# Kernel tuning notes

Measured on AMD Instinct MI355X. Metric: run time of the kernel, lower is better.

The kernel has to match this reference:

```python
import jax, jax.numpy as jnp
import numpy as np

N_USER = 100_000
N_ITEM = 50_000
C = 128
E = 600_000
L = 2          # num_layers
NN = 2         # num_layers_nn (MLP depth inside GINConv)
LN_EPS = 1e-5


def _layernorm(x, g, b):
    # PyG LayerNorm(mode='node'): normalize each node over channels, affine
    m = jnp.mean(x, axis=-1, keepdims=True)
    v = jnp.mean((x - m) ** 2, axis=-1, keepdims=True)
    return (x - m) * jax.lax.rsqrt(v + LN_EPS) * g + b


def _mlp(x, W, b):
    # GINConv inner MLP: [Linear -> ReLU] * NN
    for i in range(NN):
        x = jax.nn.relu(x @ W[i] + b[i])
    return x


def setup_inputs() -> dict:
    key = jax.random.key(0)
    ks = jax.random.split(key, 10)
    s = 1.0 / np.sqrt(C)
    edge_ui = jnp.stack([
        jax.random.randint(ks[0], (E,), 0, N_USER, dtype=jnp.int32),  # src: user
        jax.random.randint(ks[1], (E,), 0, N_ITEM, dtype=jnp.int32),  # dst: item
    ])
    edge_iu = jnp.stack([
        jax.random.randint(ks[2], (E,), 0, N_ITEM, dtype=jnp.int32),  # src: item
        jax.random.randint(ks[3], (E,), 0, N_USER, dtype=jnp.int32),  # dst: user
    ])
    return {
        "x_user": jax.random.normal(ks[4], (N_USER, C), dtype=jnp.float32),
        "x_item": jax.random.normal(ks[5], (N_ITEM, C), dtype=jnp.float32),
        "W_init": jax.random.normal(ks[6], (2, C, C), dtype=jnp.float32) * s,
        "b_init": jnp.zeros((2, C), dtype=jnp.float32),
        "mlp_W": jax.random.normal(ks[7], (L, 2, NN, C, C), dtype=jnp.float32) * s,
        "mlp_b": jnp.zeros((L, 2, NN, C), dtype=jnp.float32),
        "eps": jnp.full((L, 2), 1e-5, dtype=jnp.float32),  # train_eps=True, init eps=1e-5
        "ln_g": jnp.ones((L, 2, C), dtype=jnp.float32),
        "ln_b": jnp.zeros((L, 2, C), dtype=jnp.float32),
        "edge_ui": edge_ui,
        "edge_iu": edge_iu,
    }


def reference(x_user, x_item, W_init, b_init, mlp_W, mlp_b, eps, ln_g, ln_b,
              edge_ui, edge_iu):
    # Initial per-node-type projection (LazyLinear)
    xu = x_user @ W_init[0] + b_init[0]
    xi = x_item @ W_init[1] + b_init[1]
    for l in range(L):
        # GINConv per edge type; HeteroConv(aggr='sum') trivially reduces since
        # each node type is targeted by exactly one edge type here.
        agg_i = jax.ops.segment_sum(xu[edge_ui[0]], edge_ui[1], num_segments=N_ITEM)
        agg_u = jax.ops.segment_sum(xi[edge_iu[0]], edge_iu[1], num_segments=N_USER)
        # edge_type index 0 = (user->item), 1 = (item->user)
        new_i = _mlp((1.0 + eps[l, 0]) * xi + agg_i, mlp_W[l, 0], mlp_b[l, 0])
        new_u = _mlp((1.0 + eps[l, 1]) * xu + agg_u, mlp_W[l, 1], mlp_b[l, 1])
        # node_type index 0 = user, 1 = item
        xu = jax.nn.relu(_layernorm(new_u, ln_g[l, 0], ln_b[l, 0]))
        xi = jax.nn.relu(_layernorm(new_i, ln_g[l, 1], ln_b[l, 1]))
    return (xu, xi)
```

## Files before the change

kernel.cpp:

```cpp
#include <hip/hip_runtime.h>
#include <cstdint>
#include <cstddef>

#define N_USER 100000
#define N_ITEM 50000
#define CDIM   128
#define NEDGE  600000
#define N_SEG  (N_ITEM + N_USER)
#define NB_SCAN ((N_SEG + 255) / 256)

#define FILL_EPB 2048
#define FILL_NCHUNK ((NEDGE + FILL_EPB - 1) / FILL_EPB)
#define SLICE_DIV ((N_SEG + 7) / 8)

typedef __bf16 bf16_t;
typedef bf16_t bfvec8 __attribute__((ext_vector_type(8)));
typedef bf16_t bfvec4 __attribute__((ext_vector_type(4)));
typedef float  f32x4  __attribute__((ext_vector_type(4)));

#define LDW 136

__global__ __launch_bounds__(256) void prep_weights(
    const float* __restrict__ W_init, const float* __restrict__ mlp_W,
    bf16_t* __restrict__ wtg)
{
    int m  = blockIdx.x >> 6;
    int it = blockIdx.x & 63;
    const float* src = (m < 2) ? (W_init + (size_t)m * 16384)
                               : (mlp_W + (size_t)(m - 2) * 16384);
    int e = it * 256 + threadIdx.x;
    int n = e >> 7, k = e & 127;
    wtg[(size_t)m * 16384 + e] = (bf16_t)src[k * 128 + n];
}

template <int NT>
static __device__ inline void stage_wbf(bf16_t* Wt, const bf16_t* __restrict__ Wg, int tid) {
    #pragma unroll
    for (int c = tid; c < 2048; c += NT) {
        int n = c >> 4, koff = (c & 15) * 8;
        *reinterpret_cast<bfvec8*>(&Wt[n * LDW + koff]) =
            *reinterpret_cast<const bfvec8*>(&Wg[n * 128 + koff]);
    }
}

__global__ __launch_bounds__(512) void gemm_init(
    const float* __restrict__ X,
    const bf16_t* __restrict__ Wg,
    const float* __restrict__ B,
    bf16_t* __restrict__ Y, int M)
{
    __shared__ __align__(16) bf16_t Wt[128 * LDW];
    const int tid = threadIdx.x;
    stage_wbf<512>(Wt, Wg, tid);
    __syncthreads();

    const int wave = tid >> 6, lane = tid & 63;
    const int quad = lane >> 4, ln16 = lane & 15;
    const int row_l = wave * 16 + ln16;
    const int rowg = blockIdx.x * 128 + row_l;
    const int rowc = rowg < M ? rowg : 0;

    bfvec8 xb[4];
    const float* xp = X + (size_t)rowc * CDIM + quad * 8;
    #pragma unroll
    for (int kc = 0; kc < 4; ++kc) {
        f32x4 lo = *reinterpret_cast<const f32x4*>(xp + kc * 32);
        f32x4 hi = *reinterpret_cast<const f32x4*>(xp + kc * 32 + 4);
        #pragma unroll
        for (int j = 0; j < 4; ++j) {
            xb[kc][j]     = (bf16_t)lo[j];
            xb[kc][j + 4] = (bf16_t)hi[j];
        }
    }

    f32x4 acc[8];
    #pragma unroll
    for (int t = 0; t < 8; ++t) acc[t] = (f32x4){0.f, 0.f, 0.f, 0.f};
    #pragma unroll
    for (int t = 0; t < 8; ++t) {
        const bf16_t* wp = &Wt[(t * 16 + ln16) * LDW + quad * 8];
        #pragma unroll
        for (int kc = 0; kc < 4; ++kc) {
            bfvec8 wv = *reinterpret_cast<const bfvec8*>(wp + kc * 32);
            acc[t] = __builtin_amdgcn_mfma_f32_16x16x32_bf16(wv, xb[kc], acc[t], 0, 0, 0);
        }
    }

    if (rowg < M) {
        #pragma unroll
        for (int t = 0; t < 8; ++t) {
            f32x4 bv = *reinterpret_cast<const f32x4*>(&B[t * 16 + quad * 4]);
            bfvec4 o;
            #pragma unroll
            for (int r = 0; r < 4; ++r) o[r] = (bf16_t)(acc[t][r] + bv[r]);
            *reinterpret_cast<bfvec4*>(&Y[(size_t)rowg * CDIM + t * 16 + quad * 4]) = o;
        }
    }
}

__global__ __launch_bounds__(256) void zero_i32(int* __restrict__ p, int n)
{
    int i = blockIdx.x * 256 + threadIdx.x;
    if (i < n) p[i] = 0;
}

__global__ __launch_bounds__(256) void hist_rank(
    const int* __restrict__ edge_ui, const int* __restrict__ edge_iu,
    int* __restrict__ deg, int2* __restrict__ rank2)
{
    int i = blockIdx.x * 256 + threadIdx.x;
    if (i >= NEDGE) return;
    int r0 = atomicAdd(&deg[edge_ui[NEDGE + i]], 1);
    int r1 = atomicAdd(&deg[N_ITEM + edge_iu[NEDGE + i]], 1);
    rank2[i] = make_int2(r0, r1);
}

__global__ __launch_bounds__(256) void block_scan(
    int* __restrict__ off, int* __restrict__ bsum, int n)
{
    __shared__ int sh[256];
    int tid = threadIdx.x;
    int i = blockIdx.x * 256 + tid;
    int v = (i < n) ? off[i] : 0;
    sh[tid] = v;
    __syncthreads();
    #pragma unroll
    for (int d = 1; d < 256; d <<= 1) {
        int t = (tid >= d) ? sh[tid - d] : 0;
        __syncthreads();
        sh[tid] += t;
        __syncthreads();
    }
    if (i < n) off[i] = sh[tid] - v;
    if (tid == 255) bsum[blockIdx.x] = sh[255];
}

__global__ __launch_bounds__(1024) void scan_bsums(int* __restrict__ bsum)
{
    __shared__ int sh[1024];
    int tid = threadIdx.x;
    int v = (tid < NB_SCAN) ? bsum[tid] : 0;
    sh[tid] = v;
    __syncthreads();
    #pragma unroll
    for (int d = 1; d < 1024; d <<= 1) {
        int t = (tid >= d) ? sh[tid - d] : 0;
        __syncthreads();
        sh[tid] += t;
        __syncthreads();
    }
    if (tid < NB_SCAN) bsum[tid] = sh[tid] - v;
    if (tid == 1023) bsum[NB_SCAN] = sh[1023];
}

__global__ __launch_bounds__(256) void add_offsets(
    int* __restrict__ off, const int* __restrict__ bsum, int n)
{
    int i = blockIdx.x * 256 + threadIdx.x;
    if (i < n) off[i] += bsum[i >> 8];
    else if (i == n) off[n] = bsum[NB_SCAN];
}

__global__ __launch_bounds__(256) void fill_sliced(
    const int* __restrict__ edge_ui, const int* __restrict__ edge_iu,
    const int* __restrict__ off, const int2* __restrict__ rank2,
    int* __restrict__ srcbuf)
{
    const int r = blockIdx.x & 7;
    const int chunk = blockIdx.x >> 3;
    const int base = chunk * FILL_EPB + threadIdx.x;
    #pragma unroll
    for (int j = 0; j < FILL_EPB / 256; ++j) {
        int i = base + j * 256;
        if (i < NEDGE) {
            int d0 = edge_ui[NEDGE + i];
            int d1 = edge_iu[NEDGE + i] + N_ITEM;
            int2 rk = rank2[i];
            if (d0 / SLICE_DIV == r)
                srcbuf[off[d0] + rk.x] = edge_ui[i];
            if (d1 / SLICE_DIV == r)
                srcbuf[off[d1] + rk.y] = edge_iu[i];
        }
    }
}

__global__ __launch_bounds__(256) void gather_both(
    const bf16_t* __restrict__ xu, const bf16_t* __restrict__ xi,
    const float* __restrict__ eps2,
    const int* __restrict__ off_all, const int* __restrict__ srcbuf,
    bf16_t* __restrict__ ti, bf16_t* __restrict__ tu)
{
    const int gBI = (N_ITEM + 3) / 4;
    int b = blockIdx.x;
    bool isItem = b < gBI;
    int wave = threadIdx.x >> 6;
    int node = (isItem ? b : b - gBI) * 4 + wave;
    int n = isItem ? N_ITEM : N_USER;
    if (node >= n) return;

    const bfvec8* F = reinterpret_cast<const bfvec8*>(isItem ? xu : xi);
    const bfvec8* X = reinterpret_cast<const bfvec8*>(isItem ? xi : xu);
    const int* off = isItem ? off_all : off_all + N_ITEM;
    bfvec8* out = reinterpret_cast<bfvec8*>(isItem ? ti : tu);
    float s = 1.f + (isItem ? eps2[0] : eps2[1]);

    int lane = threadIdx.x & 63;
    int grp  = lane >> 4;
    int l16  = lane & 15;
    int start = off[node], end = off[node + 1];

    float acc[8];
    #pragma unroll
    for (int j = 0; j < 8; ++j) acc[j] = 0.f;

    int e = start + grp;
    for (; e + 12 < end; e += 16) {
        int s0 = srcbuf[e];
        int s1 = srcbuf[e + 4];
        int s2 = srcbuf[e + 8];
        int s3 = srcbuf[e + 12];
        bfvec8 v0 = F[(size_t)s0 * 16 + l16];
        bfvec8 v1 = F[(size_t)s1 * 16 + l16];
        bfvec8 v2 = F[(size_t)s2 * 16 + l16];
        bfvec8 v3 = F[(size_t)s3 * 16 + l16];
        #pragma unroll
        for (int j = 0; j < 8; ++j)
            acc[j] += ((float)v0[j] + (float)v1[j]) + ((float)v2[j] + (float)v3[j]);
    }
    for (; e + 4 < end; e += 8) {
        int s0 = srcbuf[e];
        int s1 = srcbuf[e + 4];
        bfvec8 v0 = F[(size_t)s0 * 16 + l16];
        bfvec8 v1 = F[(size_t)s1 * 16 + l16];
        #pragma unroll
        for (int j = 0; j < 8; ++j) acc[j] += (float)v0[j] + (float)v1[j];
    }
    for (; e < end; e += 4) {
        bfvec8 v = F[(size_t)srcbuf[e] * 16 + l16];
        #pragma unroll
        for (int j = 0; j < 8; ++j) acc[j] += (float)v[j];
    }

    #pragma unroll
    for (int j = 0; j < 8; ++j) {
        acc[j] += __shfl_xor(acc[j], 16, 64);
        acc[j] += __shfl_xor(acc[j], 32, 64);
    }

    if (grp == 0) {
        bfvec8 xv = X[(size_t)node * 16 + l16];
        bfvec8 o;
        #pragma unroll
        for (int j = 0; j < 8; ++j) o[j] = (bf16_t)(s * (float)xv[j] + acc[j]);
        out[(size_t)node * 16 + l16] = o;
    }
}

__global__ __launch_bounds__(512) void mlp_ln_both(
    const bf16_t* __restrict__ ti, const bf16_t* __restrict__ tu,
    const bf16_t* __restrict__ wg,
    const float* __restrict__ mlpb,
    const float* __restrict__ lng,
    const float* __restrict__ lnb,
    bf16_t* __restrict__ xib, bf16_t* __restrict__ xub,
    float* __restrict__ xif, float* __restrict__ xuf,
    int f32out)
{
    __shared__ __align__(16) bf16_t Wt[128 * LDW];
    __shared__ __align__(16) bf16_t At[128 * LDW];

    const int gBI = (N_ITEM + 127) / 128;
    int b = blockIdx.x;
    bool isItem = b < gBI;
    const bf16_t* X = isItem ? ti : tu;
    bf16_t* Yb      = isItem ? xib : xub;
    float*  Yf      = isItem ? xif : xuf;
    int M  = isItem ? N_ITEM : N_USER;
    int bx = isItem ? b : b - gBI;
    const bf16_t* W1 = wg + (isItem ? 0 : 2) * 16384;
    const bf16_t* W2 = W1 + 16384;
    const float* B1 = mlpb + (isItem ? 0 : 2) * 128;
    const float* B2 = B1 + 128;
    const float* G  = lng + (isItem ? 128 : 0);
    const float* Bb = lnb + (isItem ? 128 : 0);

    const int tid = threadIdx.x;
    stage_wbf<512>(Wt, W1, tid);
    __syncthreads();

    const int wave = tid >> 6, lane = tid & 63;
    const int quad = lane >> 4, ln16 = lane & 15;
    const int row_l = wave * 16 + ln16;
    const int rowg = bx * 128 + row_l;
    const int rowc = rowg < M ? rowg : 0;

    bfvec8 xb[4];
    const bf16_t* xp = X + (size_t)rowc * CDIM + quad * 8;
    #pragma unroll
    for (int kc = 0; kc < 4; ++kc)
        xb[kc] = *reinterpret_cast<const bfvec8*>(xp + kc * 32);

    f32x4 acc[8];
    #pragma unroll
    for (int t = 0; t < 8; ++t) acc[t] = (f32x4){0.f, 0.f, 0.f, 0.f};
    #pragma unroll
    for (int t = 0; t < 8; ++t) {
        const bf16_t* wp = &Wt[(t * 16 + ln16) * LDW + quad * 8];
        #pragma unroll
        for (int kc = 0; kc < 4; ++kc) {
            bfvec8 wv = *reinterpret_cast<const bfvec8*>(wp + kc * 32);
            acc[t] = __builtin_amdgcn_mfma_f32_16x16x32_bf16(wv, xb[kc], acc[t], 0, 0, 0);
        }
    }

    #pragma unroll
    for (int t = 0; t < 8; ++t) {
        f32x4 bv = *reinterpret_cast<const f32x4*>(&B1[t * 16 + quad * 4]);
        bfvec4 o;
        #pragma unroll
        for (int r = 0; r < 4; ++r) {
            float v = acc[t][r] + bv[r];
            o[r] = (bf16_t)(v > 0.f ? v : 0.f);
        }
        *reinterpret_cast<bfvec4*>(&At[row_l * LDW + t * 16 + quad * 4]) = o;
    }
    __syncthreads();
    stage_wbf<512>(Wt, W2, tid);
    __syncthreads();

    bfvec8 hb[4];
    #pragma unroll
    for (int kc = 0; kc < 4; ++kc)
        hb[kc] = *reinterpret_cast<const bfvec8*>(&At[row_l * LDW + kc * 32 + quad * 8]);

    #pragma unroll
    for (int t = 0; t < 8; ++t) acc[t] = (f32x4){0.f, 0.f, 0.f, 0.f};
    #pragma unroll
    for (int t = 0; t < 8; ++t) {
        const bf16_t* wp = &Wt[(t * 16 + ln16) * LDW + quad * 8];
        #pragma unroll
        for (int kc = 0; kc < 4; ++kc) {
            bfvec8 wv = *reinterpret_cast<const bfvec8*>(wp + kc * 32);
            acc[t] = __builtin_amdgcn_mfma_f32_16x16x32_bf16(wv, hb[kc], acc[t], 0, 0, 0);
        }
    }

    #pragma unroll
    for (int t = 0; t < 8; ++t) {
        f32x4 bv = *reinterpret_cast<const f32x4*>(&B2[t * 16 + quad * 4]);
        #pragma unroll
        for (int r = 0; r < 4; ++r) {
            float v = acc[t][r] + bv[r];
            acc[t][r] = v > 0.f ? v : 0.f;
        }
    }

    float sm = 0.f;
    #pragma unroll
    for (int t = 0; t < 8; ++t)
        #pragma unroll
        for (int r = 0; r < 4; ++r) sm += acc[t][r];
    sm += __shfl_xor(sm, 16, 64);
    sm += __shfl_xor(sm, 32, 64);
    float mean = sm * (1.f / 128.f);
    float sq = 0.f;
    #pragma unroll
    for (int t = 0; t < 8; ++t)
        #pragma unroll
        for (int r = 0; r < 4; ++r) { float d = acc[t][r] - mean; sq += d * d; }
    sq += __shfl_xor(sq, 16, 64);
    sq += __shfl_xor(sq, 32, 64);
    float rs = rsqrtf(sq * (1.f / 128.f) + 1e-5f);

    if (rowg < M) {
        if (f32out) {
            #pragma unroll
            for (int t = 0; t < 8; ++t) {
                f32x4 g4 = *reinterpret_cast<const f32x4*>(&G[t * 16 + quad * 4]);
                f32x4 b4 = *reinterpret_cast<const f32x4*>(&Bb[t * 16 + quad * 4]);
                f32x4 y;
                #pragma unroll
                for (int r = 0; r < 4; ++r) {
                    float v = (acc[t][r] - mean) * rs * g4[r] + b4[r];
                    y[r] = v > 0.f ? v : 0.f;
                }
                *reinterpret_cast<f32x4*>(&Yf[(size_t)rowg * CDIM + t * 16 + quad * 4]) = y;
            }
        } else {
            #pragma unroll
            for (int t = 0; t < 8; ++t) {
                f32x4 g4 = *reinterpret_cast<const f32x4*>(&G[t * 16 + quad * 4]);
                f32x4 b4 = *reinterpret_cast<const f32x4*>(&Bb[t * 16 + quad * 4]);
                bfvec4 y;
                #pragma unroll
                for (int r = 0; r < 4; ++r) {
                    float v = (acc[t][r] - mean) * rs * g4[r] + b4[r];
                    y[r] = (bf16_t)(v > 0.f ? v : 0.f);
                }
                *reinterpret_cast<bfvec4*>(&Yb[(size_t)rowg * CDIM + t * 16 + quad * 4]) = y;
            }
        }
    }
}

extern "C" void kernel_launch(void* const* d_in, const int* in_sizes, int n_in,
                              void* d_out, int out_size, void* d_ws, size_t ws_size,
                              hipStream_t stream)
{
    const float* x_user = (const float*)d_in[0];
    const float* x_item = (const float*)d_in[1];
    const float* W_init = (const float*)d_in[2];
    const float* b_init = (const float*)d_in[3];
    const float* mlp_W  = (const float*)d_in[4];
    const float* mlp_b  = (const float*)d_in[5];
    const float* eps    = (const float*)d_in[6];
    const float* ln_g   = (const float*)d_in[7];
    const float* ln_b   = (const float*)d_in[8];
    const int* edge_ui  = (const int*)d_in[9];
    const int* edge_iu  = (const int*)d_in[10];

    float* xuf = (float*)d_out;
    float* xif = xuf + (size_t)N_USER * CDIM;

    char* w = (char*)d_ws;
    bf16_t* xub = (bf16_t*)w;
    bf16_t* xib = xub + (size_t)N_USER * CDIM;
    bf16_t* tub = xib + (size_t)N_ITEM * CDIM;
    bf16_t* tib = tub + (size_t)N_USER * CDIM;
    int* off_all = (int*)(tib + (size_t)N_ITEM * CDIM);
    int* bsum    = off_all + (N_SEG + 4);
    int* srcbuf  = bsum + (NB_SCAN + 2);
    bf16_t* wtg  = (bf16_t*)(srcbuf + 2 * NEDGE);

    int2* rank2 = (int2*)tub;

    const int gU = (N_USER + 127) / 128;
    const int gI = (N_ITEM + 127) / 128;
    const int gSeg = (N_SEG + 256) / 256;
    const int gE = (NEDGE + 255) / 256;
    const int gGather = (N_ITEM + 3) / 4 + (N_USER + 3) / 4;

    prep_weights<<<640, 256, 0, stream>>>(W_init, mlp_W, wtg);

    zero_i32<<<(N_SEG + 255) / 256, 256, 0, stream>>>(off_all, N_SEG);
    hist_rank<<<gE, 256, 0, stream>>>(edge_ui, edge_iu, off_all, rank2);
    block_scan<<<NB_SCAN, 256, 0, stream>>>(off_all, bsum, N_SEG);
    scan_bsums<<<1, 1024, 0, stream>>>(bsum);
    add_offsets<<<gSeg, 256, 0, stream>>>(off_all, bsum, N_SEG);
    fill_sliced<<<FILL_NCHUNK * 8, 256, 0, stream>>>(edge_ui, edge_iu, off_all, rank2, srcbuf);

    gemm_init<<<gU, 512, 0, stream>>>(x_user, wtg,         b_init,       xub, N_USER);
    gemm_init<<<gI, 512, 0, stream>>>(x_item, wtg + 16384, b_init + 128, xib, N_ITEM);

    for (int l = 0; l < 2; ++l) {
        gather_both<<<gGather, 256, 0, stream>>>(
            xub, xib, eps + 2 * l, off_all, srcbuf, tib, tub);
        mlp_ln_both<<<gI + gU, 512, 0, stream>>>(
            tib, tub, wtg + (size_t)(2 + l * 4) * 16384, mlp_b + l * 4 * 128,
            ln_g + l * 2 * 128, ln_b + l * 2 * 128,
            xib, xub, xif, xuf, (l == 1) ? 1 : 0);
    }
}
```

Measured before the change: 467.7 us.

## Fuse neighbor gather into MLP+LayerNorm kernel via shared-memory staging

Merges the per-node gather/aggregation kernel into the MLP+LayerNorm kernel. Each 128-row block now gathers its own rows' neighbor sums directly into the shared-memory A tile before the MFMA GEMMs, and uses ping-pong buffers across the two layers. This removes the intermediate bf16 write and re-read of the aggregated features and two kernel launches. The cost is that each wave now walks 16 nodes serially with less parallelism and memory-level overlap than the old one-node-per-wave launch, and the 512-thread blocks carry the larger shared footprint during the latency-bound gather phase.

```diff
diff --git a/kernel.cpp b/kernel.cpp
--- a/kernel.cpp
+++ b/kernel.cpp
@@ -184,85 +184,15 @@
     }
 }
 
-__global__ __launch_bounds__(256) void gather_both(
-    const bf16_t* __restrict__ xu, const bf16_t* __restrict__ xi,
+__global__ __launch_bounds__(512) void gin_layer(
+    const bf16_t* __restrict__ xu_in, const bf16_t* __restrict__ xi_in,
     const float* __restrict__ eps2,
     const int* __restrict__ off_all, const int* __restrict__ srcbuf,
-    bf16_t* __restrict__ ti, bf16_t* __restrict__ tu)
-{
-    const int gBI = (N_ITEM + 3) / 4;
-    int b = blockIdx.x;
-    bool isItem = b < gBI;
-    int wave = threadIdx.x >> 6;
-    int node = (isItem ? b : b - gBI) * 4 + wave;
-    int n = isItem ? N_ITEM : N_USER;
-    if (node >= n) return;
-
-    const bfvec8* F = reinterpret_cast<const bfvec8*>(isItem ? xu : xi);
-    const bfvec8* X = reinterpret_cast<const bfvec8*>(isItem ? xi : xu);
-    const int* off = isItem ? off_all : off_all + N_ITEM;
-    bfvec8* out = reinterpret_cast<bfvec8*>(isItem ? ti : tu);
-    float s = 1.f + (isItem ? eps2[0] : eps2[1]);
-
-    int lane = threadIdx.x & 63;
-    int grp  = lane >> 4;
-    int l16  = lane & 15;
-    int start = off[node], end = off[node + 1];
-
-    float acc[8];
-    #pragma unroll
-    for (int j = 0; j < 8; ++j) acc[j] = 0.f;
-
-    int e = start + grp;
-    for (; e + 12 < end; e += 16) {
-        int s0 = srcbuf[e];
-        int s1 = srcbuf[e + 4];
-        int s2 = srcbuf[e + 8];
-        int s3 = srcbuf[e + 12];
-        bfvec8 v0 = F[(size_t)s0 * 16 + l16];
-        bfvec8 v1 = F[(size_t)s1 * 16 + l16];
-        bfvec8 v2 = F[(size_t)s2 * 16 + l16];
-        bfvec8 v3 = F[(size_t)s3 * 16 + l16];
-        #pragma unroll
-        for (int j = 0; j < 8; ++j)
-            acc[j] += ((float)v0[j] + (float)v1[j]) + ((float)v2[j] + (float)v3[j]);
-    }
-    for (; e + 4 < end; e += 8) {
-        int s0 = srcbuf[e];
-        int s1 = srcbuf[e + 4];
-        bfvec8 v0 = F[(size_t)s0 * 16 + l16];
-        bfvec8 v1 = F[(size_t)s1 * 16 + l16];
-        #pragma unroll
-        for (int j = 0; j < 8; ++j) acc[j] += (float)v0[j] + (float)v1[j];
-    }
-    for (; e < end; e += 4) {
-        bfvec8 v = F[(size_t)srcbuf[e] * 16 + l16];
-        #pragma unroll
-        for (int j = 0; j < 8; ++j) acc[j] += (float)v[j];
-    }
-
-    #pragma unroll
-    for (int j = 0; j < 8; ++j) {
-        acc[j] += __shfl_xor(acc[j], 16, 64);
-        acc[j] += __shfl_xor(acc[j], 32, 64);
-    }
-
-    if (grp == 0) {
-        bfvec8 xv = X[(size_t)node * 16 + l16];
-        bfvec8 o;
-        #pragma unroll
-        for (int j = 0; j < 8; ++j) o[j] = (bf16_t)(s * (float)xv[j] + acc[j]);
-        out[(size_t)node * 16 + l16] = o;
-    }
-}
-
-__global__ __launch_bounds__(512) void mlp_ln_both(
-    const bf16_t* __restrict__ ti, const bf16_t* __restrict__ tu,
     const bf16_t* __restrict__ wg,
     const float* __restrict__ mlpb,
     const float* __restrict__ lng,
     const float* __restrict__ lnb,
-    bf16_t* __restrict__ xib, bf16_t* __restrict__ xub,
+    bf16_t* __restrict__ yib, bf16_t* __restrict__ yub,
     float* __restrict__ xif, float* __restrict__ xuf,
     int f32out)
 {
@@ -272,11 +202,16 @@
     const int gBI = (N_ITEM + 127) / 128;
     int b = blockIdx.x;
     bool isItem = b < gBI;
-    const bf16_t* X = isItem ? ti : tu;
-    bf16_t* Yb      = isItem ? xib : xub;
-    float*  Yf      = isItem ? xif : xuf;
     int M  = isItem ? N_ITEM : N_USER;
     int bx = isItem ? b : b - gBI;
+
+    const bfvec8* F = reinterpret_cast<const bfvec8*>(isItem ? xu_in : xi_in);
+    const bfvec8* X = reinterpret_cast<const bfvec8*>(isItem ? xi_in : xu_in);
+    const int* off = isItem ? off_all : off_all + N_ITEM;
+    bf16_t* Yb     = isItem ? yib : yub;
+    float*  Yf     = isItem ? xif : xuf;
+    float s = 1.f + (isItem ? eps2[0] : eps2[1]);
+
     const bf16_t* W1 = wg + (isItem ? 0 : 2) * 16384;
     const bf16_t* W2 = W1 + 16384;
     const float* B1 = mlpb + (isItem ? 0 : 2) * 128;
@@ -286,19 +221,77 @@
 
     const int tid = threadIdx.x;
     stage_wbf<512>(Wt, W1, tid);
-    __syncthreads();
 
     const int wave = tid >> 6, lane = tid & 63;
     const int quad = lane >> 4, ln16 = lane & 15;
+    const int rowBase = bx * 128;
+
+    for (int rr = 0; rr < 16; ++rr) {
+        int rowl = wave * 16 + rr;
+        int node = rowBase + rowl;
+        float acc[8];
+        #pragma unroll
+        for (int j = 0; j < 8; ++j) acc[j] = 0.f;
+
+        if (node < M) {
+            int start = off[node], end = off[node + 1];
+            int e = start + quad;
+            for (; e + 12 < end; e += 16) {
+                int s0 = srcbuf[e];
+                int s1 = srcbuf[e + 4];
+                int s2 = srcbuf[e + 8];
+                int s3 = srcbuf[e + 12];
+                bfvec8 v0 = F[(size_t)s0 * 16 + ln16];
+                bfvec8 v1 = F[(size_t)s1 * 16 + ln16];
+                bfvec8 v2 = F[(size_t)s2 * 16 + ln16];
+                bfvec8 v3 = F[(size_t)s3 * 16 + ln16];
+                #pragma unroll
+                for (int j = 0; j < 8; ++j)
+                    acc[j] += ((float)v0[j] + (float)v1[j]) + ((float)v2[j] + (float)v3[j]);
+            }
+            for (; e + 4 < end; e += 8) {
+                int s0 = srcbuf[e];
+                int s1 = srcbuf[e + 4];
+                bfvec8 v0 = F[(size_t)s0 * 16 + ln16];
+                bfvec8 v1 = F[(size_t)s1 * 16 + ln16];
+                #pragma unroll
+                for (int j = 0; j < 8; ++j) acc[j] += (float)v0[j] + (float)v1[j];
+            }
+            for (; e < end; e += 4) {
+                bfvec8 v = F[(size_t)srcbuf[e] * 16 + ln16];
+                #pragma unroll
+                for (int j = 0; j < 8; ++j) acc[j] += (float)v[j];
+            }
+        }
+
+        #pragma unroll
+        for (int j = 0; j < 8; ++j) {
+            acc[j] += __shfl_xor(acc[j], 16, 64);
+            acc[j] += __shfl_xor(acc[j], 32, 64);
+        }
+
+        if (quad == 0) {
+            bfvec8 o;
+            if (node < M) {
+                bfvec8 xv = X[(size_t)node * 16 + ln16];
+                #pragma unroll
+                for (int j = 0; j < 8; ++j) o[j] = (bf16_t)(s * (float)xv[j] + acc[j]);
+            } else {
+                #pragma unroll
+                for (int j = 0; j < 8; ++j) o[j] = (bf16_t)0.f;
+            }
+            *reinterpret_cast<bfvec8*>(&At[rowl * LDW + ln16 * 8]) = o;
+        }
+    }
+    __syncthreads();
+
     const int row_l = wave * 16 + ln16;
-    const int rowg = bx * 128 + row_l;
-    const int rowc = rowg < M ? rowg : 0;
+    const int rowg = rowBase + row_l;
 
     bfvec8 xb[4];
-    const bf16_t* xp = X + (size_t)rowc * CDIM + quad * 8;
     #pragma unroll
     for (int kc = 0; kc < 4; ++kc)
-        xb[kc] = *reinterpret_cast<const bfvec8*>(xp + kc * 32);
+        xb[kc] = *reinterpret_cast<const bfvec8*>(&At[row_l * LDW + kc * 32 + quad * 8]);
 
     f32x4 acc[8];
     #pragma unroll
@@ -438,7 +431,6 @@
     const int gI = (N_ITEM + 127) / 128;
     const int gSeg = (N_SEG + 256) / 256;
     const int gE = (NEDGE + 255) / 256;
-    const int gGather = (N_ITEM + 3) / 4 + (N_USER + 3) / 4;
 
     prep_weights<<<640, 256, 0, stream>>>(W_init, mlp_W, wtg);
 
@@ -452,12 +444,12 @@
     gemm_init<<<gU, 512, 0, stream>>>(x_user, wtg,         b_init,       xub, N_USER);
     gemm_init<<<gI, 512, 0, stream>>>(x_item, wtg + 16384, b_init + 128, xib, N_ITEM);
 
-    for (int l = 0; l < 2; ++l) {
-        gather_both<<<gGather, 256, 0, stream>>>(
-            xub, xib, eps + 2 * l, off_all, srcbuf, tib, tub);
-        mlp_ln_both<<<gI + gU, 512, 0, stream>>>(
-            tib, tub, wtg + (size_t)(2 + l * 4) * 16384, mlp_b + l * 4 * 128,
-            ln_g + l * 2 * 128, ln_b + l * 2 * 128,
-            xib, xub, xif, xuf, (l == 1) ? 1 : 0);
-    }
-}
+    gin_layer<<<gI + gU, 512, 0, stream>>>(
+        xub, xib, eps, off_all, srcbuf,
+        wtg + (size_t)2 * 16384, mlp_b, ln_g, ln_b,
+        tib, tub, xif, xuf, 0);
+    gin_layer<<<gI + gU, 512, 0, stream>>>(
+        tub, tib, eps + 2, off_all, srcbuf,
+        wtg + (size_t)6 * 16384, mlp_b + 4 * 128, ln_g + 2 * 128, ln_b + 2 * 128,
+        nullptr, nullptr, xif, xuf, 1);
+}
```

Result: slower. 692.7 us (+48.1%).

## Fuse init GEMM with histogram and overlap gathers with MLP via role-split kernels

Applied to the files above, without the earlier changes.

Merges the initial projection GEMMs and the edge histogram into one launch with block roles. It reorders the layer schedule so the item-side MLP runs in the same kernel as the next layer's gather, using role-dispatched blocks. The self term (1+eps)*x moves from the gather into the MLP load. The MLP reuses a single shared-memory buffer for the hidden activations and second weight, which halves LDS and allows higher occupancy (launch bounds 512,6). The last user-side aggregate is staged in fp32 inside the output buffer and overwritten in place, which adds some complexity and extra syncs.

```diff
diff --git a/kernel.cpp b/kernel.cpp
--- a/kernel.cpp
+++ b/kernel.cpp
@@ -8,6 +8,12 @@
 #define NEDGE  600000
 #define N_SEG  (N_ITEM + N_USER)
 #define NB_SCAN ((N_SEG + 255) / 256)
+
+#define GU 782
+#define GI 391
+#define GHIST ((NEDGE + 511) / 512)
+#define GBI8 (N_ITEM / 8)
+#define GBU8 (N_USER / 8)
 
 #define FILL_EPB 2048
 #define FILL_NCHUNK ((NEDGE + FILL_EPB - 1) / FILL_EPB)
@@ -43,21 +49,17 @@
     }
 }
 
-__global__ __launch_bounds__(512) void gemm_init(
-    const float* __restrict__ X,
-    const bf16_t* __restrict__ Wg,
-    const float* __restrict__ B,
-    bf16_t* __restrict__ Y, int M)
-{
-    __shared__ __align__(16) bf16_t Wt[128 * LDW];
-    const int tid = threadIdx.x;
+static __device__ inline void gemm_init_role(
+    bf16_t* Wt, const float* __restrict__ X, const bf16_t* __restrict__ Wg,
+    const float* __restrict__ B, bf16_t* __restrict__ Y, int M, int rowBase, int tid)
+{
     stage_wbf<512>(Wt, Wg, tid);
     __syncthreads();
 
     const int wave = tid >> 6, lane = tid & 63;
     const int quad = lane >> 4, ln16 = lane & 15;
     const int row_l = wave * 16 + ln16;
-    const int rowg = blockIdx.x * 128 + row_l;
+    const int rowg = rowBase + row_l;
     const int rowc = rowg < M ? rowg : 0;
 
     bfvec8 xb[4];
@@ -98,21 +100,33 @@
     }
 }
 
+__global__ __launch_bounds__(512) void fuse_a(
+    const float* __restrict__ x_user, const float* __restrict__ x_item,
+    const bf16_t* __restrict__ wtg, const float* __restrict__ b_init,
+    bf16_t* __restrict__ xub, bf16_t* __restrict__ xib,
+    const int* __restrict__ edge_ui, const int* __restrict__ edge_iu,
+    int* __restrict__ deg, int2* __restrict__ rank2)
+{
+    __shared__ __align__(16) bf16_t Wt[128 * LDW];
+    int b = blockIdx.x, tid = threadIdx.x;
+    if (b < GU) {
+        gemm_init_role(Wt, x_user, wtg, b_init, xub, N_USER, b * 128, tid);
+    } else if (b < GU + GI) {
+        gemm_init_role(Wt, x_item, wtg + 16384, b_init + 128, xib, N_ITEM, (b - GU) * 128, tid);
+    } else {
+        int i = (b - GU - GI) * 512 + tid;
+        if (i < NEDGE) {
+            int r0 = atomicAdd(&deg[edge_ui[NEDGE + i]], 1);
+            int r1 = atomicAdd(&deg[N_ITEM + edge_iu[NEDGE + i]], 1);
+            rank2[i] = make_int2(r0, r1);
+        }
+    }
+}
+
 __global__ __launch_bounds__(256) void zero_i32(int* __restrict__ p, int n)
 {
     int i = blockIdx.x * 256 + threadIdx.x;
     if (i < n) p[i] = 0;
-}
-
-__global__ __launch_bounds__(256) void hist_rank(
-    const int* __restrict__ edge_ui, const int* __restrict__ edge_iu,
-    int* __restrict__ deg, int2* __restrict__ rank2)
-{
-    int i = blockIdx.x * 256 + threadIdx.x;
-    if (i >= NEDGE) return;
-    int r0 = atomicAdd(&deg[edge_ui[NEDGE + i]], 1);
-    int r1 = atomicAdd(&deg[N_ITEM + edge_iu[NEDGE + i]], 1);
-    rank2[i] = make_int2(r0, r1);
 }
 
 __global__ __launch_bounds__(256) void block_scan(
@@ -184,31 +198,18 @@
     }
 }
 
-__global__ __launch_bounds__(256) void gather_both(
-    const bf16_t* __restrict__ xu, const bf16_t* __restrict__ xi,
-    const float* __restrict__ eps2,
-    const int* __restrict__ off_all, const int* __restrict__ srcbuf,
-    bf16_t* __restrict__ ti, bf16_t* __restrict__ tu)
-{
-    const int gBI = (N_ITEM + 3) / 4;
-    int b = blockIdx.x;
-    bool isItem = b < gBI;
-    int wave = threadIdx.x >> 6;
-    int node = (isItem ? b : b - gBI) * 4 + wave;
-    int n = isItem ? N_ITEM : N_USER;
-    if (node >= n) return;
-
-    const bfvec8* F = reinterpret_cast<const bfvec8*>(isItem ? xu : xi);
-    const bfvec8* X = reinterpret_cast<const bfvec8*>(isItem ? xi : xu);
-    const int* off = isItem ? off_all : off_all + N_ITEM;
-    bfvec8* out = reinterpret_cast<bfvec8*>(isItem ? ti : tu);
-    float s = 1.f + (isItem ? eps2[0] : eps2[1]);
-
-    int lane = threadIdx.x & 63;
-    int grp  = lane >> 4;
-    int l16  = lane & 15;
+static __device__ inline void gather_role(
+    const bfvec8* __restrict__ F, const int* __restrict__ off,
+    const int* __restrict__ srcbuf,
+    bf16_t* __restrict__ outB, float* __restrict__ outF, int f32out,
+    int M, int nodeBase, int tid)
+{
+    int wave = tid >> 6, lane = tid & 63;
+    int grp = lane >> 4, l16 = lane & 15;
+    int node = nodeBase + wave;
+    if (node >= M) return;
+
     int start = off[node], end = off[node + 1];
-
     float acc[8];
     #pragma unroll
     for (int j = 0; j < 8; ++j) acc[j] = 0.f;
@@ -248,57 +249,61 @@
     }
 
     if (grp == 0) {
-        bfvec8 xv = X[(size_t)node * 16 + l16];
-        bfvec8 o;
-        #pragma unroll
-        for (int j = 0; j < 8; ++j) o[j] = (bf16_t)(s * (float)xv[j] + acc[j]);
-        out[(size_t)node * 16 + l16] = o;
-    }
-}
-
-__global__ __launch_bounds__(512) void mlp_ln_both(
-    const bf16_t* __restrict__ ti, const bf16_t* __restrict__ tu,
-    const bf16_t* __restrict__ wg,
-    const float* __restrict__ mlpb,
-    const float* __restrict__ lng,
-    const float* __restrict__ lnb,
-    bf16_t* __restrict__ xib, bf16_t* __restrict__ xub,
-    float* __restrict__ xif, float* __restrict__ xuf,
-    int f32out)
-{
-    __shared__ __align__(16) bf16_t Wt[128 * LDW];
-    __shared__ __align__(16) bf16_t At[128 * LDW];
-
-    const int gBI = (N_ITEM + 127) / 128;
-    int b = blockIdx.x;
-    bool isItem = b < gBI;
-    const bf16_t* X = isItem ? ti : tu;
-    bf16_t* Yb      = isItem ? xib : xub;
-    float*  Yf      = isItem ? xif : xuf;
-    int M  = isItem ? N_ITEM : N_USER;
-    int bx = isItem ? b : b - gBI;
-    const bf16_t* W1 = wg + (isItem ? 0 : 2) * 16384;
-    const bf16_t* W2 = W1 + 16384;
-    const float* B1 = mlpb + (isItem ? 0 : 2) * 128;
-    const float* B2 = B1 + 128;
-    const float* G  = lng + (isItem ? 128 : 0);
-    const float* Bb = lnb + (isItem ? 128 : 0);
-
-    const int tid = threadIdx.x;
-    stage_wbf<512>(Wt, W1, tid);
+        if (f32out) {
+            f32x4 lo = (f32x4){acc[0], acc[1], acc[2], acc[3]};
+            f32x4 hi = (f32x4){acc[4], acc[5], acc[6], acc[7]};
+            float* p = outF + (size_t)node * CDIM + l16 * 8;
+            *reinterpret_cast<f32x4*>(p)     = lo;
+            *reinterpret_cast<f32x4*>(p + 4) = hi;
+        } else {
+            bfvec8 o;
+            #pragma unroll
+            for (int j = 0; j < 8; ++j) o[j] = (bf16_t)acc[j];
+            reinterpret_cast<bfvec8*>(outB)[(size_t)node * 16 + l16] = o;
+        }
+    }
+}
+
+static __device__ inline void mlp_role(
+    bf16_t* Wt, int tid, int rowBase, int M,
+    const bf16_t* __restrict__ AggB, const float* __restrict__ AggF, int aggF32,
+    const bf16_t* __restrict__ Xself, const float* __restrict__ epsp,
+    const bf16_t* __restrict__ W1g, const bf16_t* __restrict__ W2g,
+    const float* __restrict__ B1, const float* __restrict__ B2,
+    const float* __restrict__ G, const float* __restrict__ Bb,
+    bf16_t* __restrict__ Yb, float* __restrict__ Yf, int f32out)
+{
+    stage_wbf<512>(Wt, W1g, tid);
     __syncthreads();
 
     const int wave = tid >> 6, lane = tid & 63;
     const int quad = lane >> 4, ln16 = lane & 15;
     const int row_l = wave * 16 + ln16;
-    const int rowg = bx * 128 + row_l;
+    const int rowg = rowBase + row_l;
     const int rowc = rowg < M ? rowg : 0;
+    const float s = 1.f + epsp[0];
 
     bfvec8 xb[4];
-    const bf16_t* xp = X + (size_t)rowc * CDIM + quad * 8;
-    #pragma unroll
-    for (int kc = 0; kc < 4; ++kc)
-        xb[kc] = *reinterpret_cast<const bfvec8*>(xp + kc * 32);
+    const bf16_t* xp = Xself + (size_t)rowc * CDIM + quad * 8;
+    #pragma unroll
+    for (int kc = 0; kc < 4; ++kc) {
+        bfvec8 xv = *reinterpret_cast<const bfvec8*>(xp + kc * 32);
+        float av[8];
+        if (aggF32) {
+            const float* ap = AggF + (size_t)rowc * CDIM + kc * 32 + quad * 8;
+            f32x4 lo = *reinterpret_cast<const f32x4*>(ap);
+            f32x4 hi = *reinterpret_cast<const f32x4*>(ap + 4);
+            #pragma unroll
+            for (int j = 0; j < 4; ++j) { av[j] = lo[j]; av[j + 4] = hi[j]; }
+        } else {
+            bfvec8 ab = *reinterpret_cast<const bfvec8*>(
+                AggB + (size_t)rowc * CDIM + kc * 32 + quad * 8);
+            #pragma unroll
+            for (int j = 0; j < 8; ++j) av[j] = (float)ab[j];
+        }
+        #pragma unroll
+        for (int j = 0; j < 8; ++j) xb[kc][j] = (bf16_t)(s * (float)xv[j] + av[j]);
+    }
 
     f32x4 acc[8];
     #pragma unroll
@@ -312,6 +317,7 @@
             acc[t] = __builtin_amdgcn_mfma_f32_16x16x32_bf16(wv, xb[kc], acc[t], 0, 0, 0);
         }
     }
+    __syncthreads();
 
     #pragma unroll
     for (int t = 0; t < 8; ++t) {
@@ -322,16 +328,18 @@
             float v = acc[t][r] + bv[r];
             o[r] = (bf16_t)(v > 0.f ? v : 0.f);
         }
-        *reinterpret_cast<bfvec4*>(&At[row_l * LDW + t * 16 + quad * 4]) = o;
-    }
-    __syncthreads();
-    stage_wbf<512>(Wt, W2, tid);
+        *reinterpret_cast<bfvec4*>(&Wt[row_l * LDW + t * 16 + quad * 4]) = o;
+    }
     __syncthreads();
 
     bfvec8 hb[4];
     #pragma unroll
     for (int kc = 0; kc < 4; ++kc)
-        hb[kc] = *reinterpret_cast<const bfvec8*>(&At[row_l * LDW + kc * 32 + quad * 8]);
+        hb[kc] = *reinterpret_cast<const bfvec8*>(&Wt[row_l * LDW + kc * 32 + quad * 8]);
+    __syncthreads();
+
+    stage_wbf<512>(Wt, W2g, tid);
+    __syncthreads();
 
     #pragma unroll
     for (int t = 0; t < 8; ++t) acc[t] = (f32x4){0.f, 0.f, 0.f, 0.f};
@@ -403,6 +411,74 @@
     }
 }
 
+__global__ __launch_bounds__(512) void gather0(
+    const bf16_t* __restrict__ xub, const bf16_t* __restrict__ xib,
+    const int* __restrict__ off_all, const int* __restrict__ srcbuf,
+    bf16_t* __restrict__ tib, bf16_t* __restrict__ tub)
+{
+    int b = blockIdx.x, tid = threadIdx.x;
+    if (b < GBI8)
+        gather_role(reinterpret_cast<const bfvec8*>(xub), off_all, srcbuf,
+                    tib, nullptr, 0, N_ITEM, b * 8, tid);
+    else
+        gather_role(reinterpret_cast<const bfvec8*>(xib), off_all + N_ITEM, srcbuf,
+                    tub, nullptr, 0, N_USER, (b - GBI8) * 8, tid);
+}
+
+__global__ __launch_bounds__(512, 6) void mlp_k(
+    const bf16_t* __restrict__ AggB, const float* __restrict__ AggF, int aggF32,
+    const bf16_t* __restrict__ Xself, const float* __restrict__ epsp,
+    const bf16_t* __restrict__ W1g, const bf16_t* __restrict__ W2g,
+    const float* __restrict__ B1, const float* __restrict__ B2,
+    const float* __restrict__ G, const float* __restrict__ Bb,
+    bf16_t* __restrict__ Yb, float* __restrict__ Yf, int f32out, int M)
+{
+    __shared__ __align__(16) bf16_t Wt[128 * LDW];
+    mlp_role(Wt, threadIdx.x, blockIdx.x * 128, M, AggB, AggF, aggF32,
+             Xself, epsp, W1g, W2g, B1, B2, G, Bb, Yb, Yf, f32out);
+}
+
+__global__ __launch_bounds__(512, 6) void fuse_b(
+    const bf16_t* __restrict__ tib, const bf16_t* __restrict__ xib_in,
+    bf16_t* __restrict__ xib_out,
+    const bf16_t* __restrict__ xub,
+    const float* __restrict__ epsp,
+    const bf16_t* __restrict__ W1g, const bf16_t* __restrict__ W2g,
+    const float* __restrict__ B1, const float* __restrict__ B2,
+    const float* __restrict__ G, const float* __restrict__ Bb,
+    const int* __restrict__ off_all, const int* __restrict__ srcbuf,
+    bf16_t* __restrict__ t1i)
+{
+    __shared__ __align__(16) bf16_t Wt[128 * LDW];
+    int b = blockIdx.x, tid = threadIdx.x;
+    if (b < GI)
+        mlp_role(Wt, tid, b * 128, N_ITEM, tib, nullptr, 0, xib_in, epsp,
+                 W1g, W2g, B1, B2, G, Bb, xib_out, nullptr, 0);
+    else
+        gather_role(reinterpret_cast<const bfvec8*>(xub), off_all, srcbuf,
+                    t1i, nullptr, 0, N_ITEM, (b - GI) * 8, tid);
+}
+
+__global__ __launch_bounds__(512, 6) void fuse_c(
+    const bf16_t* __restrict__ t1i, const bf16_t* __restrict__ xib,
+    float* __restrict__ xif,
+    const float* __restrict__ epsp,
+    const bf16_t* __restrict__ W1g, const bf16_t* __restrict__ W2g,
+    const float* __restrict__ B1, const float* __restrict__ B2,
+    const float* __restrict__ G, const float* __restrict__ Bb,
+    const int* __restrict__ off_all, const int* __restrict__ srcbuf,
+    float* __restrict__ xuf_agg)
+{
+    __shared__ __align__(16) bf16_t Wt[128 * LDW];
+    int b = blockIdx.x, tid = threadIdx.x;
+    if (b < GI)
+        mlp_role(Wt, tid, b * 128, N_ITEM, t1i, nullptr, 0, xib, epsp,
+                 W1g, W2g, B1, B2, G, Bb, nullptr, xif, 1);
+    else
+        gather_role(reinterpret_cast<const bfvec8*>(xib), off_all + N_ITEM, srcbuf,
+                    nullptr, xuf_agg, 1, N_USER, (b - GI) * 8, tid);
+}
+
 extern "C" void kernel_launch(void* const* d_in, const int* in_sizes, int n_in,
                               void* d_out, int out_size, void* d_ws, size_t ws_size,
                               hipStream_t stream)
@@ -434,30 +510,46 @@
 
     int2* rank2 = (int2*)tub;
 
-    const int gU = (N_USER + 127) / 128;
-    const int gI = (N_ITEM + 127) / 128;
     const int gSeg = (N_SEG + 256) / 256;
-    const int gE = (NEDGE + 255) / 256;
-    const int gGather = (N_ITEM + 3) / 4 + (N_USER + 3) / 4;
+
+    const bf16_t* Wi0_1 = wtg + (size_t)2 * 16384;
+    const bf16_t* Wi0_2 = wtg + (size_t)3 * 16384;
+    const bf16_t* Wu0_1 = wtg + (size_t)4 * 16384;
+    const bf16_t* Wu0_2 = wtg + (size_t)5 * 16384;
+    const bf16_t* Wi1_1 = wtg + (size_t)6 * 16384;
+    const bf16_t* Wi1_2 = wtg + (size_t)7 * 16384;
+    const bf16_t* Wu1_1 = wtg + (size_t)8 * 16384;
+    const bf16_t* Wu1_2 = wtg + (size_t)9 * 16384;
 
     prep_weights<<<640, 256, 0, stream>>>(W_init, mlp_W, wtg);
-
     zero_i32<<<(N_SEG + 255) / 256, 256, 0, stream>>>(off_all, N_SEG);
-    hist_rank<<<gE, 256, 0, stream>>>(edge_ui, edge_iu, off_all, rank2);
+
+    fuse_a<<<GU + GI + GHIST, 512, 0, stream>>>(
+        x_user, x_item, wtg, b_init, xub, xib, edge_ui, edge_iu, off_all, rank2);
+
     block_scan<<<NB_SCAN, 256, 0, stream>>>(off_all, bsum, N_SEG);
     scan_bsums<<<1, 1024, 0, stream>>>(bsum);
     add_offsets<<<gSeg, 256, 0, stream>>>(off_all, bsum, N_SEG);
     fill_sliced<<<FILL_NCHUNK * 8, 256, 0, stream>>>(edge_ui, edge_iu, off_all, rank2, srcbuf);
 
-    gemm_init<<<gU, 512, 0, stream>>>(x_user, wtg,         b_init,       xub, N_USER);
-    gemm_init<<<gI, 512, 0, stream>>>(x_item, wtg + 16384, b_init + 128, xib, N_ITEM);
-
-    for (int l = 0; l < 2; ++l) {
-        gather_both<<<gGather, 256, 0, stream>>>(
-            xub, xib, eps + 2 * l, off_all, srcbuf, tib, tub);
-        mlp_ln_both<<<gI + gU, 512, 0, stream>>>(
-            tib, tub, wtg + (size_t)(2 + l * 4) * 16384, mlp_b + l * 4 * 128,
-            ln_g + l * 2 * 128, ln_b + l * 2 * 128,
-            xib, xub, xif, xuf, (l == 1) ? 1 : 0);
-    }
-}
+    gather0<<<GBI8 + GBU8, 512, 0, stream>>>(xub, xib, off_all, srcbuf, tib, tub);
+
+    mlp_k<<<GU, 512, 0, stream>>>(
+        tub, nullptr, 0, xub, eps + 1, Wu0_1, Wu0_2,
+        mlp_b + 256, mlp_b + 384, ln_g, ln_b, xub, nullptr, 0, N_USER);
+
+    fuse_b<<<GI + GBI8, 512, 0, stream>>>(
+        tib, xib, xib, xub, eps + 0, Wi0_1, Wi0_2,
+        mlp_b + 0, mlp_b + 128, ln_g + 128, ln_b + 128,
+        off_all, srcbuf, tub);
+
+    fuse_c<<<GI + GBU8, 512, 0, stream>>>(
+        tub, xib, xif, eps + 2, Wi1_1, Wi1_2,
+        mlp_b + 512, mlp_b + 640, ln_g + 384, ln_b + 384,
+        off_all, srcbuf, xuf);
+
+    mlp_k<<<GU, 512, 0, stream>>>(
+        nullptr, xuf, 1, xub, eps + 3, Wu1_1, Wu1_2,
+        mlp_b + 768, mlp_b + 896, ln_g + 256, ln_b + 256,
+        nullptr, xuf, 1, N_USER);
+}
```

New measurement: 626.2 us. 33.9% more time.

## Split gather into channel chunks and alias MLP hidden tile onto weight smem

Applied to the files above, without the earlier changes.

The gather is restructured so each block handles one quarter of the channel width (32 channels) for four nodes. Sixteen edge groups per wave each load 16-byte pieces, and four channel-chunk blocks are interleaved in the grid, presumably to make each chunk's working set of source features friendlier to cache. The MLP kernel drops its separate activation shared-memory tile: it writes the hidden layer into the weight buffer, reads it back into registers, then restages W2, with a 6-blocks hint in launch bounds. This adds more reductions and barriers in exchange for lower LDS use and higher occupancy.

```diff
diff --git a/kernel.cpp b/kernel.cpp
--- a/kernel.cpp
+++ b/kernel.cpp
@@ -12,6 +12,9 @@
 #define FILL_EPB 2048
 #define FILL_NCHUNK ((NEDGE + FILL_EPB - 1) / FILL_EPB)
 #define SLICE_DIV ((N_SEG + 7) / 8)
+
+#define GCH_IDX 25000
+#define GCH (8 * GCH_IDX)
 
 typedef __bf16 bf16_t;
 typedef bf16_t bfvec8 __attribute__((ext_vector_type(8)));
@@ -184,19 +187,21 @@
     }
 }
 
-__global__ __launch_bounds__(256) void gather_both(
+__global__ __launch_bounds__(256) void gather_chunk(
     const bf16_t* __restrict__ xu, const bf16_t* __restrict__ xi,
     const float* __restrict__ eps2,
     const int* __restrict__ off_all, const int* __restrict__ srcbuf,
     bf16_t* __restrict__ ti, bf16_t* __restrict__ tu)
 {
-    const int gBI = (N_ITEM + 3) / 4;
     int b = blockIdx.x;
-    bool isItem = b < gBI;
+    int slot = b & 7, idx = b >> 3;
+    bool isItem = slot < 4;
+    if (isItem && idx >= 12500) return;
+    int chunk = isItem ? slot : slot - 4;
     int wave = threadIdx.x >> 6;
-    int node = (isItem ? b : b - gBI) * 4 + wave;
-    int n = isItem ? N_ITEM : N_USER;
-    if (node >= n) return;
+    int node = idx * 4 + wave;
+    int M = isItem ? N_ITEM : N_USER;
+    if (node >= M) return;
 
     const bfvec8* F = reinterpret_cast<const bfvec8*>(isItem ? xu : xi);
     const bfvec8* X = reinterpret_cast<const bfvec8*>(isItem ? xi : xu);
@@ -205,58 +210,38 @@
     float s = 1.f + (isItem ? eps2[0] : eps2[1]);
 
     int lane = threadIdx.x & 63;
-    int grp  = lane >> 4;
-    int l16  = lane & 15;
+    int grp = lane >> 2, l4 = lane & 3;
+    int cbase = chunk * 4 + l4;
     int start = off[node], end = off[node + 1];
 
     float acc[8];
     #pragma unroll
     for (int j = 0; j < 8; ++j) acc[j] = 0.f;
 
-    int e = start + grp;
-    for (; e + 12 < end; e += 16) {
-        int s0 = srcbuf[e];
-        int s1 = srcbuf[e + 4];
-        int s2 = srcbuf[e + 8];
-        int s3 = srcbuf[e + 12];
-        bfvec8 v0 = F[(size_t)s0 * 16 + l16];
-        bfvec8 v1 = F[(size_t)s1 * 16 + l16];
-        bfvec8 v2 = F[(size_t)s2 * 16 + l16];
-        bfvec8 v3 = F[(size_t)s3 * 16 + l16];
-        #pragma unroll
-        for (int j = 0; j < 8; ++j)
-            acc[j] += ((float)v0[j] + (float)v1[j]) + ((float)v2[j] + (float)v3[j]);
-    }
-    for (; e + 4 < end; e += 8) {
-        int s0 = srcbuf[e];
-        int s1 = srcbuf[e + 4];
-        bfvec8 v0 = F[(size_t)s0 * 16 + l16];
-        bfvec8 v1 = F[(size_t)s1 * 16 + l16];
-        #pragma unroll
-        for (int j = 0; j < 8; ++j) acc[j] += (float)v0[j] + (float)v1[j];
-    }
-    for (; e < end; e += 4) {
-        bfvec8 v = F[(size_t)srcbuf[e] * 16 + l16];
+    for (int e = start + grp; e < end; e += 16) {
+        bfvec8 v = F[(size_t)srcbuf[e] * 16 + cbase];
         #pragma unroll
         for (int j = 0; j < 8; ++j) acc[j] += (float)v[j];
     }
 
     #pragma unroll
     for (int j = 0; j < 8; ++j) {
+        acc[j] += __shfl_xor(acc[j], 4, 64);
+        acc[j] += __shfl_xor(acc[j], 8, 64);
         acc[j] += __shfl_xor(acc[j], 16, 64);
         acc[j] += __shfl_xor(acc[j], 32, 64);
     }
 
     if (grp == 0) {
-        bfvec8 xv = X[(size_t)node * 16 + l16];
+        bfvec8 xv = X[(size_t)node * 16 + cbase];
         bfvec8 o;
         #pragma unroll
         for (int j = 0; j < 8; ++j) o[j] = (bf16_t)(s * (float)xv[j] + acc[j]);
-        out[(size_t)node * 16 + l16] = o;
-    }
-}
-
-__global__ __launch_bounds__(512) void mlp_ln_both(
+        out[(size_t)node * 16 + cbase] = o;
+    }
+}
+
+__global__ __launch_bounds__(512, 6) void mlp_ln_both(
     const bf16_t* __restrict__ ti, const bf16_t* __restrict__ tu,
     const bf16_t* __restrict__ wg,
     const float* __restrict__ mlpb,
@@ -267,7 +252,6 @@
     int f32out)
 {
     __shared__ __align__(16) bf16_t Wt[128 * LDW];
-    __shared__ __align__(16) bf16_t At[128 * LDW];
 
     const int gBI = (N_ITEM + 127) / 128;
     int b = blockIdx.x;
@@ -312,6 +296,7 @@
             acc[t] = __builtin_amdgcn_mfma_f32_16x16x32_bf16(wv, xb[kc], acc[t], 0, 0, 0);
         }
     }
+    __syncthreads();
 
     #pragma unroll
     for (int t = 0; t < 8; ++t) {
@@ -322,16 +307,18 @@
             float v = acc[t][r] + bv[r];
             o[r] = (bf16_t)(v > 0.f ? v : 0.f);
         }
-        *reinterpret_cast<bfvec4*>(&At[row_l * LDW + t * 16 + quad * 4]) = o;
-    }
-    __syncthreads();
+        *reinterpret_cast<bfvec4*>(&Wt[row_l * LDW + t * 16 + quad * 4]) = o;
+    }
+    __syncthreads();
+
+    bfvec8 hb[4];
+    #pragma unroll
+    for (int kc = 0; kc < 4; ++kc)
+        hb[kc] = *reinterpret_cast<const bfvec8*>(&Wt[row_l * LDW + kc * 32 + quad * 8]);
+    __syncthreads();
+
     stage_wbf<512>(Wt, W2, tid);
     __syncthreads();
-
-    bfvec8 hb[4];
-    #pragma unroll
-    for (int kc = 0; kc < 4; ++kc)
-        hb[kc] = *reinterpret_cast<const bfvec8*>(&At[row_l * LDW + kc * 32 + quad * 8]);
 
     #pragma unroll
     for (int t = 0; t < 8; ++t) acc[t] = (f32x4){0.f, 0.f, 0.f, 0.f};
@@ -438,7 +425,6 @@
     const int gI = (N_ITEM + 127) / 128;
     const int gSeg = (N_SEG + 256) / 256;
     const int gE = (NEDGE + 255) / 256;
-    const int gGather = (N_ITEM + 3) / 4 + (N_USER + 3) / 4;
 
     prep_weights<<<640, 256, 0, stream>>>(W_init, mlp_W, wtg);
 
@@ -453,7 +439,7 @@
     gemm_init<<<gI, 512, 0, stream>>>(x_item, wtg + 16384, b_init + 128, xib, N_ITEM);
 
     for (int l = 0; l < 2; ++l) {
-        gather_both<<<gGather, 256, 0, stream>>>(
+        gather_chunk<<<GCH, 256, 0, stream>>>(
             xub, xib, eps + 2 * l, off_all, srcbuf, tib, tub);
         mlp_ln_both<<<gI + gU, 512, 0, stream>>>(
             tib, tub, wtg + (size_t)(2 + l * 4) * 16384, mlp_b + l * 4 * 128,
```

Result: slower. 859.8 us (+83.8%).
